# Kernel optimization log

Measured on AMD Instinct MI355X. Metric: run time of the kernel, lower is better.

Reference implementation:

```python
import jax, jax.numpy as jnp
import numpy as np
import math

# D4 group multiplication permutations (rows of the 8x8 regular representation)
PERMS = (
    (0, 1, 2, 3, 4, 5, 6, 7),
    (3, 0, 1, 2, 5, 6, 7, 4),
    (2, 3, 0, 1, 6, 7, 4, 5),
    (1, 2, 3, 0, 7, 4, 5, 6),
    (4, 5, 6, 7, 0, 1, 2, 3),
    (5, 6, 7, 4, 3, 0, 1, 2),
    (6, 7, 4, 5, 2, 3, 0, 1),
    (7, 4, 5, 6, 1, 2, 3, 0),
)


def d4_1x1(x, w):
    """D4-equivariant 1x1 conv. x: (b, cin*8, h, w), w: (cout, cin, 8)."""
    b, C, h, ww = x.shape
    cout, cin, _ = w.shape
    # (cout, 8, cin, 8): permuted copies of the base weight
    W = jnp.stack([w[..., jnp.array(p)] for p in PERMS], axis=1)
    xr = x.reshape(b, cin, 8, h, ww)
    y = jnp.einsum('ogif,bifhw->boghw', W, xr)
    return y.reshape(b, cout * 8, h, ww)


def group_norm(x, gamma, beta, num_groups, eps=1e-5):
    b, C, h, w = x.shape
    xg = x.reshape(b, num_groups, C // num_groups, h, w)
    mean = xg.mean(axis=(2, 3, 4), keepdims=True)
    var = xg.var(axis=(2, 3, 4), keepdims=True)
    xn = ((xg - mean) / jnp.sqrt(var + eps)).reshape(b, C, h, w)
    return xn * gamma[None, :, None, None] + beta[None, :, None, None]


def unfold_patches(x, k):
    """torch.nn.Unfold(k, 1, (k-1)//2, 1) -> (b, C, k*k, h, w), patch idx = ki*k+kj."""
    b, C, h, w = x.shape
    p = (k - 1) // 2
    xp = jnp.pad(x, ((0, 0), (0, 0), (p, p), (p, p)))
    pats = jnp.stack([xp[:, :, i:i + h, j:j + w]
                      for i in range(k) for j in range(k)], axis=2)
    return pats


def setup_inputs() -> dict:
    key = jax.random.key(0)
    ks = jax.random.split(key, 4)
    b, H, W = 8, 56, 56
    cin, cout, rr, k, gc = 64, 64, 2, 3, 16
    cmid = cin // rr            # 32
    G = cout // gc              # 4 dynamic-kernel groups
    x = jax.random.normal(ks[0], (b, cin * 8, H, W), jnp.float32)
    w_v = jax.random.normal(ks[1], (cout, cin, 8), jnp.float32) / math.sqrt(8 * cin / 2)
    w1 = jax.random.normal(ks[2], (cmid, cin, 8), jnp.float32) / math.sqrt(8 * cin / 2)
    gn_gamma = jnp.ones((cmid * 8,), jnp.float32)
    gn_beta = jnp.zeros((cmid * 8,), jnp.float32)
    w2 = jax.random.normal(ks[3], (k * k * G, cmid), jnp.float32) / math.sqrt(cmid)
    b2 = jnp.zeros((k * k * G,), jnp.float32)
    return {"x": x, "w_v": w_v, "w1": w1, "gn_gamma": gn_gamma,
            "gn_beta": gn_beta, "w2": w2, "b2": b2}


def reference(x, w_v, w1, gn_gamma, gn_beta, w2, b2):
    k, gc = 3, 16
    b, _, h, w = x.shape
    cmid = w1.shape[0]
    G = w2.shape[0] // (k * k)
    # --- dynamic kernel branch: conv1 (D4 1x1 + GN + ReLU), conv2 (1x1x1 conv3d)
    t = jax.nn.relu(group_norm(d4_1x1(x, w1), gn_gamma, gn_beta, cmid))
    tr = t.reshape(b, cmid, 8, h, w)
    wgt = jnp.einsum('oi,bighw->boghw', w2, tr) + b2[None, :, None, None, None]
    wv = wgt.reshape(b, G, k, k, 8, h, w)
    # --- D4 symmetrization of the k x k kernel per group element
    s = [wv[:, :, :, :, g] for g in range(8)]          # each (b,G,k,k,h,w)
    sw = [jnp.swapaxes(s[g], 2, 3) for g in range(4, 8)]
    trans = [s[0],
             jnp.rot90(s[1], 1, (2, 3)),
             jnp.rot90(s[2], 2, (2, 3)),
             jnp.rot90(s[3], 3, (2, 3)),
             jnp.rot90(sw[0], 3, (2, 3)),
             jnp.rot90(sw[1], 2, (2, 3)),
             jnp.rot90(sw[2], 1, (2, 3)),
             sw[3]]
    wv = jnp.stack(trans, axis=4)                      # (b,G,k,k,8,h,w)
    wv = wv.reshape(b, G, k * k, 8, h, w)[:, :, None]  # (b,G,1,k^2,8,h,w)
    wv = jnp.swapaxes(wv, 3, 4)                        # (b,G,1,8,k^2,h,w)
    # --- value branch + unfold + multiply-sum
    xv = d4_1x1(x, w_v)                                # (b, cout*8, h, w)
    pats = unfold_patches(xv, k).reshape(b, G, gc, 8, k * k, h, w)
    out = (wv * pats).sum(axis=4)                      # (b,G,gc,8,h,w)
    return out.reshape(b, G * gc * 8, h, w)
```

## Files before the change

kernel.cpp:

```cpp
#include <hip/hip_runtime.h>

#define BATCH 8
#define PIX   3136
#define CIN8  512
#define CMID8 256
#define KDIM  512

typedef short short8 __attribute__((ext_vector_type(8)));
typedef float f32x4 __attribute__((ext_vector_type(4)));

__constant__ int c_perms[8][8] = {
    {0, 1, 2, 3, 4, 5, 6, 7},
    {3, 0, 1, 2, 5, 6, 7, 4},
    {2, 3, 0, 1, 6, 7, 4, 5},
    {1, 2, 3, 0, 7, 4, 5, 6},
    {4, 5, 6, 7, 0, 1, 2, 3},
    {5, 6, 7, 4, 3, 0, 1, 2},
    {6, 7, 4, 5, 2, 3, 0, 1},
};
__constant__ int c_perm7[8] = {7, 4, 5, 6, 1, 2, 3, 0};

__constant__ int c_tab[8][9] = {
    {0, 1, 2, 3, 4, 5, 6, 7, 8},
    {2, 5, 8, 1, 4, 7, 0, 3, 6},
    {8, 7, 6, 5, 4, 3, 2, 1, 0},
    {6, 3, 0, 7, 4, 1, 8, 5, 2},
    {2, 1, 0, 5, 4, 3, 8, 7, 6},
    {8, 5, 2, 7, 4, 1, 6, 3, 0},
    {6, 7, 8, 3, 4, 5, 0, 1, 2},
    {0, 3, 6, 1, 4, 7, 2, 5, 8},
};

__device__ __forceinline__ float bf2f(unsigned short u) {
    union { unsigned int i; float f; } v;
    v.i = ((unsigned int)u) << 16;
    return v.f;
}
__device__ __forceinline__ unsigned short f2bf(float f) {
    union { float f; unsigned int u; } v;
    v.f = f;
    unsigned int u = v.u;
    u += 0x7FFFu + ((u >> 16) & 1u);
    return (unsigned short)(u >> 16);
}
__device__ __forceinline__ float bflo(unsigned int u) {
    union { unsigned int i; float f; } v; v.i = u << 16; return v.f;
}
__device__ __forceinline__ float bfhi(unsigned int u) {
    union { unsigned int i; float f; } v; v.i = u & 0xFFFF0000u; return v.f;
}

__device__ __forceinline__ void gload_lds16(const unsigned short* g, unsigned short* l) {
    __builtin_amdgcn_global_load_lds(
        (const __attribute__((address_space(1))) unsigned int*)g,
        (__attribute__((address_space(3))) unsigned int*)l,
        16, 0, 0);
}

#define LDT 70
__global__ __launch_bounds__(256) void cvt_t_kernel(
    const float* __restrict__ x, unsigned short* __restrict__ xbfT)
{
    __shared__ unsigned short T[64 * LDT];
    const int flat = blockIdx.x;
    const int kt = flat & 7;
    const int pt = (flat >> 3) % 49;
    const int b  = flat / (49 * 8);
    const int k0 = kt * 64, p0 = pt * 64;

    const float* xb = x + ((size_t)b * CIN8 + k0) * PIX + p0;
    const int kl = threadIdx.x >> 4;
    const int pl = (threadIdx.x & 15) * 4;
#pragma unroll
    for (int pass = 0; pass < 4; ++pass) {
        int kk = kl + pass * 16;
        float4 v = *(const float4*)(xb + (size_t)kk * PIX + pl);
        ushort2 lo = {f2bf(v.x), f2bf(v.y)};
        ushort2 hi = {f2bf(v.z), f2bf(v.w)};
        *(ushort2*)&T[kk * LDT + pl]     = lo;
        *(ushort2*)&T[kk * LDT + pl + 2] = hi;
    }
    __syncthreads();
    const int prow = threadIdx.x >> 2;
    const int kc8  = (threadIdx.x & 3) * 8;
    unsigned short* ob = xbfT + ((size_t)b * PIX + p0 + prow) * KDIM + k0;
#pragma unroll
    for (int pass = 0; pass < 2; ++pass) {
        int kk = kc8 + pass * 32;
        unsigned short tmp[8];
#pragma unroll
        for (int j = 0; j < 8; ++j) tmp[j] = T[(kk + j) * LDT + prow];
        *(uint4*)(ob + kk) = *(const uint4*)tmp;
    }
}

__global__ __launch_bounds__(256) void build_w_kernel(
    const float* __restrict__ w_v, const float* __restrict__ w1,
    unsigned short* __restrict__ Wbig, float* __restrict__ stats2)
{
    if (blockIdx.x < 2) stats2[blockIdx.x * 256 + threadIdx.x] = 0.f;

    int idx = blockIdx.x * 256 + threadIdx.x;
    int r = idx >> 9;
    int k = idx & 511;
    int i = k >> 3, f = k & 7;
    float v;
    if (r < 512) {
        int o = r >> 3, g = r & 7;
        int pf = (g < 7) ? c_perms[g][f] : c_perm7[f];
        v = w_v[(o * 64 + i) * 8 + pf];
    } else {
        int rr = r - 512;
        int o = rr >> 3, g = rr & 7;
        int pf = (g < 7) ? c_perms[g][f] : c_perm7[f];
        v = w1[(o * 64 + i) * 8 + pf];
    }
    Wbig[idx] = f2bf(v);
}

__global__ __launch_bounds__(256, 4) void gemm_kernel(
    const unsigned short* __restrict__ xT,
    const unsigned short* __restrict__ Wbig,
    unsigned short* __restrict__ xv,
    unsigned short* __restrict__ y1b,
    float* __restrict__ stats2)
{
    __shared__ unsigned short Wt[128 * 64];
    __shared__ unsigned short Xt[128 * 64];

    const int swz = (blockIdx.x & 7) * 147 + (blockIdx.x >> 3);
    const int rt  = swz % 6;
    const int pt  = swz / 6;
    const int row0 = rt * 128;
    const int P0   = pt * 128;

    const int tid  = threadIdx.x;
    const int lane = tid & 63;
    const int wave = tid >> 6;
    const int wm   = wave & 1;
    const int wn   = wave >> 1;

    f32x4 acc[4][4];
#pragma unroll
    for (int i = 0; i < 4; ++i)
#pragma unroll
        for (int j = 0; j < 4; ++j) acc[i][j] = (f32x4){0.f, 0.f, 0.f, 0.f};

    const int lr  = lane >> 3;
    const int lc  = lane & 7;
    const int swc = ((lc ^ lr) * 8);
    const unsigned short* wsrc = Wbig + (size_t)(row0 + wave * 32 + lr) * KDIM + swc;
    const unsigned short* xsrc = xT + (size_t)(P0 + wave * 32 + lr) * KDIM + swc;
    unsigned short* wdst = &Wt[(wave * 32) * 64];
    unsigned short* xdst = &Xt[(wave * 32) * 64];

    const int m16 = lane & 15;
    const int lq  = lane >> 4;
    const int swr = m16 & 7;

    for (int kc = 0; kc < 8; ++kc) {
        const int k0 = kc * 64;
#pragma unroll
        for (int i = 0; i < 4; ++i) {
            gload_lds16(wsrc + (size_t)i * 8 * KDIM + k0, wdst + i * 512);
            gload_lds16(xsrc + (size_t)i * 8 * KDIM + k0, xdst + i * 512);
        }
        __syncthreads();

#pragma unroll
        for (int kk = 0; kk < 2; ++kk) {
            const int ck = (((kk << 2) | lq) ^ swr) * 8;
            short8 bfrag[4];
#pragma unroll
            for (int nt = 0; nt < 4; ++nt)
                bfrag[nt] = *(const short8*)&Xt[(wn * 64 + nt * 16 + m16) * 64 + ck];
#pragma unroll
            for (int mt = 0; mt < 4; ++mt) {
                short8 afrag = *(const short8*)&Wt[(wm * 64 + mt * 16 + m16) * 64 + ck];
#pragma unroll
                for (int nt = 0; nt < 4; ++nt)
                    acc[mt][nt] = __builtin_amdgcn_mfma_f32_16x16x32_bf16(
                        afrag, bfrag[nt], acc[mt][nt], 0, 0, 0);
            }
        }
        __syncthreads();
    }

    const int colw = P0 + wn * 64;
    const int bb   = colw / PIX;
    const int pq   = colw - bb * PIX;
    const int qm   = lq * 4;

    if (row0 < 512) {
        unsigned short* dst0 = xv + ((size_t)bb * CIN8) * PIX + pq + m16;
#pragma unroll
        for (int nt = 0; nt < 4; ++nt) {
            unsigned short* dst = dst0 + nt * 16;
#pragma unroll
            for (int mt = 0; mt < 4; ++mt) {
                const int m = row0 + wm * 64 + mt * 16 + qm;
#pragma unroll
                for (int r = 0; r < 4; ++r)
                    dst[(size_t)(m + r) * PIX] = f2bf(acc[mt][nt][r]);
            }
        }
    } else {
        unsigned short* dst0 = y1b + ((size_t)bb * CMID8) * PIX + pq + m16;
#pragma unroll
        for (int nt = 0; nt < 4; ++nt) {
            unsigned short* dst = dst0 + nt * 16;
#pragma unroll
            for (int mt = 0; mt < 4; ++mt) {
                const int m = (row0 - 512) + wm * 64 + mt * 16 + qm;
#pragma unroll
                for (int r = 0; r < 4; ++r)
                    dst[(size_t)(m + r) * PIX] = f2bf(acc[mt][nt][r]);
            }
        }
        const int gbase = ((row0 - 512) + wm * 64) >> 3;
#pragma unroll
        for (int mt = 0; mt < 4; ++mt) {
            float s = 0.f, ss = 0.f;
#pragma unroll
            for (int nt = 0; nt < 4; ++nt)
#pragma unroll
                for (int r = 0; r < 4; ++r) {
                    float v = acc[mt][nt][r];
                    s += v; ss += v * v;
                }
#pragma unroll
            for (int off = 1; off <= 16; off <<= 1) {
                s  += __shfl_xor(s, off);
                ss += __shfl_xor(ss, off);
            }
            if ((lane & 31) == 0) {
                const int g = gbase + 2 * mt + (lane >> 5);
                atomicAdd(&stats2[(bb * 32 + g) * 2],     s);
                atomicAdd(&stats2[(bb * 32 + g) * 2 + 1], ss);
            }
        }
    }
}

__global__ __launch_bounds__(256) void final_fused_kernel(
    const unsigned short* __restrict__ y1b, const float* __restrict__ stats2,
    const float* __restrict__ gamma, const float* __restrict__ beta,
    const float* __restrict__ w2, const float* __restrict__ b2,
    const unsigned short* __restrict__ xv,
    float* __restrict__ out)
{
    const int swz  = (blockIdx.x & 7) * 128 + (blockIdx.x >> 3);
    const int combo = swz >> 2;
    const int b    = combo >> 5;
    const int g    = (combo >> 2) & 7;
    const int gidx = combo & 3;

    __shared__ float w2s[9 * 32];
    __shared__ float b2s9[9];
    __shared__ float scs[32], shs[32];
    const int tid = threadIdx.x;
    for (int i = tid; i < 288; i += 256) {
        int tt = i >> 5, ic = i & 31;
        w2s[i] = w2[(gidx * 9 + c_tab[g][tt]) * 32 + ic];
    }
    if (tid < 9) b2s9[tid] = b2[gidx * 9 + c_tab[g][tid]];
    if (tid < 32) {
        float S  = stats2[(b * 32 + tid) * 2];
        float SS = stats2[(b * 32 + tid) * 2 + 1];
        float mean = S * (1.f / 25088.f);
        float var  = SS * (1.f / 25088.f) - mean * mean;
        float rstd = rsqrtf(var + 1e-5f);
        float sc = rstd * gamma[tid * 8 + g];
        scs[tid] = sc;
        shs[tid] = beta[tid * 8 + g] - mean * sc;
    }
    __syncthreads();

    const int pp = (swz & 3) * 256 + tid;
    if (pp >= 784) return;
    const int p0 = pp * 4;
    const int h  = p0 / 56;
    const int w0 = p0 % 56;

    float wt[4][9];
#pragma unroll
    for (int i = 0; i < 4; ++i)
#pragma unroll
        for (int tt = 0; tt < 9; ++tt) wt[i][tt] = b2s9[tt];

    const unsigned short* yb = y1b + ((size_t)b * CMID8 + g) * PIX + p0;
#pragma unroll 4
    for (int ic = 0; ic < 32; ++ic) {
        uint2 u = *(const uint2*)(yb + (size_t)(ic * 8) * PIX);
        float t0 = bflo(u.x) * scs[ic] + shs[ic]; t0 = t0 > 0.f ? t0 : 0.f;
        float t1 = bfhi(u.x) * scs[ic] + shs[ic]; t1 = t1 > 0.f ? t1 : 0.f;
        float t2 = bflo(u.y) * scs[ic] + shs[ic]; t2 = t2 > 0.f ? t2 : 0.f;
        float t3 = bfhi(u.y) * scs[ic] + shs[ic]; t3 = t3 > 0.f ? t3 : 0.f;
#pragma unroll
        for (int tt = 0; tt < 9; ++tt) {
            float wv = w2s[tt * 32 + ic];
            wt[0][tt] = fmaf(wv, t0, wt[0][tt]);
            wt[1][tt] = fmaf(wv, t1, wt[1][tt]);
            wt[2][tt] = fmaf(wv, t2, wt[2][tt]);
            wt[3][tt] = fmaf(wv, t3, wt[3][tt]);
        }
    }

    int rb[3];
#pragma unroll
    for (int ki = 0; ki < 3; ++ki) {
        int hh = h + ki - 1;
        bool rv = (hh >= 0) & (hh < 56);
        int hc = hh < 0 ? 0 : (hh > 55 ? 55 : hh);
        rb[ki] = hc * 56;
        if (!rv) {
#pragma unroll
            for (int i = 0; i < 4; ++i)
#pragma unroll
                for (int kj = 0; kj < 3; ++kj) wt[i][ki * 3 + kj] = 0.f;
        }
    }
#pragma unroll
    for (int i = 0; i < 4; ++i)
#pragma unroll
        for (int tt = 0; tt < 9; ++tt) {
            int ww = w0 + i + (tt % 3) - 1;
            if (ww < 0 || ww >= 56) wt[i][tt] = 0.f;
        }

    const int c0 = (w0 == 0) ? 0 : (w0 - 2);

    const unsigned short* xc = xv + ((size_t)b * CIN8 + gidx * 128 + g) * PIX;
    float* ob = out + ((size_t)b * CIN8 + gidx * 128 + g) * PIX + p0;
#pragma unroll 2
    for (int cc = 0; cc < 16; ++cc) {
        f32x4 a = (f32x4){0.f, 0.f, 0.f, 0.f};
#pragma unroll
        for (int ki = 0; ki < 3; ++ki) {
            const unsigned short* row = xc + rb[ki];
            unsigned int u0 = *(const unsigned int*)(row + c0);
            unsigned int u1 = *(const unsigned int*)(row + w0);
            unsigned int u2 = *(const unsigned int*)(row + w0 + 2);
            unsigned int u3 = *(const unsigned int*)(row + w0 + 4);
            float f1 = bfhi(u0);
            float f2 = bflo(u1), f3 = bfhi(u1);
            float f4 = bflo(u2), f5 = bfhi(u2);
            float f6 = bflo(u3);
            const int t0i = ki * 3;
            a[0] = fmaf(wt[0][t0i + 0], f1, a[0]);
            a[0] = fmaf(wt[0][t0i + 1], f2, a[0]);
            a[0] = fmaf(wt[0][t0i + 2], f3, a[0]);
            a[1] = fmaf(wt[1][t0i + 0], f2, a[1]);
            a[1] = fmaf(wt[1][t0i + 1], f3, a[1]);
            a[1] = fmaf(wt[1][t0i + 2], f4, a[1]);
            a[2] = fmaf(wt[2][t0i + 0], f3, a[2]);
            a[2] = fmaf(wt[2][t0i + 1], f4, a[2]);
            a[2] = fmaf(wt[2][t0i + 2], f5, a[2]);
            a[3] = fmaf(wt[3][t0i + 0], f4, a[3]);
            a[3] = fmaf(wt[3][t0i + 1], f5, a[3]);
            a[3] = fmaf(wt[3][t0i + 2], f6, a[3]);
        }
        *(f32x4*)(ob + (size_t)cc * 8 * PIX) = a;
        xc += (size_t)8 * PIX;
    }
}

extern "C" void kernel_launch(void* const* d_in, const int* in_sizes, int n_in,
                              void* d_out, int out_size, void* d_ws, size_t ws_size,
                              hipStream_t stream) {
    (void)in_sizes; (void)n_in; (void)out_size; (void)ws_size;
    const float* x     = (const float*)d_in[0];
    const float* w_v   = (const float*)d_in[1];
    const float* w1    = (const float*)d_in[2];
    const float* gamma = (const float*)d_in[3];
    const float* beta  = (const float*)d_in[4];
    const float* w2    = (const float*)d_in[5];
    const float* b2    = (const float*)d_in[6];
    float* out = (float*)d_out;

    char* ws = (char*)d_ws;
    unsigned short* Wbig = (unsigned short*)ws;
    unsigned short* xbfT = (unsigned short*)(ws + 786432);
    unsigned short* xv   = (unsigned short*)(ws + 26476544);
    unsigned short* y1b  = (unsigned short*)(ws + 52166656);
    float* stats2 = (float*)(ws + 65011712);

    cvt_t_kernel<<<3136, 256, 0, stream>>>(x, xbfT);
    build_w_kernel<<<1536, 256, 0, stream>>>(w_v, w1, Wbig, stats2);
    gemm_kernel<<<1176, 256, 0, stream>>>(xbfT, Wbig, xv, y1b, stats2);
    final_fused_kernel<<<256 * 4, 256, 0, stream>>>(
        y1b, stats2, gamma, beta, w2, b2, xv, out);
}
```

Baseline: 160.3 us.

## Fuse fp32-to-bf16 transpose of x into GEMM tile loading

Drops the standalone convert/transpose kernel. The GEMM now loads fp32 x directly, converts it to bf16 in registers and writes it transposed into swizzled LDS. This avoids a separate kernel launch and the write and re-read of a bf16 transposed copy of x. In exchange, the GEMM reads twice the bytes per tile, repeated across row tiles, and uses synchronous loads instead of async global-to-LDS loads for that operand.

```diff
diff --git a/kernel.cpp b/kernel.cpp
--- a/kernel.cpp
+++ b/kernel.cpp
@@ -55,43 +55,6 @@
         (const __attribute__((address_space(1))) unsigned int*)g,
         (__attribute__((address_space(3))) unsigned int*)l,
         16, 0, 0);
-}
-
-#define LDT 70
-__global__ __launch_bounds__(256) void cvt_t_kernel(
-    const float* __restrict__ x, unsigned short* __restrict__ xbfT)
-{
-    __shared__ unsigned short T[64 * LDT];
-    const int flat = blockIdx.x;
-    const int kt = flat & 7;
-    const int pt = (flat >> 3) % 49;
-    const int b  = flat / (49 * 8);
-    const int k0 = kt * 64, p0 = pt * 64;
-
-    const float* xb = x + ((size_t)b * CIN8 + k0) * PIX + p0;
-    const int kl = threadIdx.x >> 4;
-    const int pl = (threadIdx.x & 15) * 4;
-#pragma unroll
-    for (int pass = 0; pass < 4; ++pass) {
-        int kk = kl + pass * 16;
-        float4 v = *(const float4*)(xb + (size_t)kk * PIX + pl);
-        ushort2 lo = {f2bf(v.x), f2bf(v.y)};
-        ushort2 hi = {f2bf(v.z), f2bf(v.w)};
-        *(ushort2*)&T[kk * LDT + pl]     = lo;
-        *(ushort2*)&T[kk * LDT + pl + 2] = hi;
-    }
-    __syncthreads();
-    const int prow = threadIdx.x >> 2;
-    const int kc8  = (threadIdx.x & 3) * 8;
-    unsigned short* ob = xbfT + ((size_t)b * PIX + p0 + prow) * KDIM + k0;
-#pragma unroll
-    for (int pass = 0; pass < 2; ++pass) {
-        int kk = kc8 + pass * 32;
-        unsigned short tmp[8];
-#pragma unroll
-        for (int j = 0; j < 8; ++j) tmp[j] = T[(kk + j) * LDT + prow];
-        *(uint4*)(ob + kk) = *(const uint4*)tmp;
-    }
 }
 
 __global__ __launch_bounds__(256) void build_w_kernel(
@@ -119,7 +82,7 @@
 }
 
 __global__ __launch_bounds__(256, 4) void gemm_kernel(
-    const unsigned short* __restrict__ xT,
+    const float* __restrict__ x,
     const unsigned short* __restrict__ Wbig,
     unsigned short* __restrict__ xv,
     unsigned short* __restrict__ y1b,
@@ -150,9 +113,19 @@
     const int lc  = lane & 7;
     const int swc = ((lc ^ lr) * 8);
     const unsigned short* wsrc = Wbig + (size_t)(row0 + wave * 32 + lr) * KDIM + swc;
-    const unsigned short* xsrc = xT + (size_t)(P0 + wave * 32 + lr) * KDIM + swc;
     unsigned short* wdst = &Wt[(wave * 32) * 64];
-    unsigned short* xdst = &Xt[(wave * 32) * 64];
+
+    const int kb = tid & 7;
+    const int pb = tid >> 3;
+    const int colx = P0 + pb * 4;
+    const int bx = colx / PIX;
+    const int px = colx - bx * PIX;
+    const float* xpA = x + ((size_t)bx * CIN8 + kb * 4) * PIX + px;
+    const float* xpB = xpA + (size_t)32 * PIX;
+    const int rowp = pb * 4;
+    const int cA = kb >> 1;
+    const int cB = (kb >> 1) + 4;
+    const int sub4 = (kb & 1) * 4;
 
     const int m16 = lane & 15;
     const int lq  = lane >> 4;
@@ -161,9 +134,26 @@
     for (int kc = 0; kc < 8; ++kc) {
         const int k0 = kc * 64;
 #pragma unroll
-        for (int i = 0; i < 4; ++i) {
+        for (int i = 0; i < 4; ++i)
             gload_lds16(wsrc + (size_t)i * 8 * KDIM + k0, wdst + i * 512);
-            gload_lds16(xsrc + (size_t)i * 8 * KDIM + k0, xdst + i * 512);
+        f32x4 xa[4], xb[4];
+#pragma unroll
+        for (int i = 0; i < 4; ++i)
+            xa[i] = *(const f32x4*)(xpA + (size_t)(k0 + i) * PIX);
+#pragma unroll
+        for (int i = 0; i < 4; ++i)
+            xb[i] = *(const f32x4*)(xpB + (size_t)(k0 + i) * PIX);
+#pragma unroll
+        for (int j = 0; j < 4; ++j) {
+            const int row = rowp + j;
+            const int rx  = row & 7;
+            unsigned int lo, hi;
+            lo = (unsigned int)f2bf(xa[0][j]) | ((unsigned int)f2bf(xa[1][j]) << 16);
+            hi = (unsigned int)f2bf(xa[2][j]) | ((unsigned int)f2bf(xa[3][j]) << 16);
+            *(uint2*)&Xt[row * 64 + (cA ^ rx) * 8 + sub4] = (uint2){lo, hi};
+            lo = (unsigned int)f2bf(xb[0][j]) | ((unsigned int)f2bf(xb[1][j]) << 16);
+            hi = (unsigned int)f2bf(xb[2][j]) | ((unsigned int)f2bf(xb[3][j]) << 16);
+            *(uint2*)&Xt[row * 64 + (cB ^ rx) * 8 + sub4] = (uint2){lo, hi};
         }
         __syncthreads();
 
@@ -380,14 +370,12 @@
 
     char* ws = (char*)d_ws;
     unsigned short* Wbig = (unsigned short*)ws;
-    unsigned short* xbfT = (unsigned short*)(ws + 786432);
-    unsigned short* xv   = (unsigned short*)(ws + 26476544);
-    unsigned short* y1b  = (unsigned short*)(ws + 52166656);
-    float* stats2 = (float*)(ws + 65011712);
-
-    cvt_t_kernel<<<3136, 256, 0, stream>>>(x, xbfT);
+    unsigned short* xv   = (unsigned short*)(ws + 786432);
+    unsigned short* y1b  = (unsigned short*)(ws + 26476544);
+    float* stats2 = (float*)(ws + 39321600);
+
     build_w_kernel<<<1536, 256, 0, stream>>>(w_v, w1, Wbig, stats2);
-    gemm_kernel<<<1176, 256, 0, stream>>>(xbfT, Wbig, xv, y1b, stats2);
+    gemm_kernel<<<1176, 256, 0, stream>>>(x, Wbig, xv, y1b, stats2);
     final_fused_kernel<<<256 * 4, 256, 0, stream>>>(
         y1b, stats2, gamma, beta, w2, b2, xv, out);
 }
```

Result: slower. 186.5 us (+16.4%).

## Double-buffer value-branch rows in LDS with async global-to-LDS prefetch

Applied to the files above, without the earlier changes.

The final fused kernel now stages each channel's needed row band of the value tensor (the block's rows plus a one-row halo) into a double-buffered shared-memory tile. It uses async global-to-LDS loads, prefetching the next channel while the current one is computed. The 3x3 neighbourhood reads then come from LDS instead of repeated, partly redundant global loads. The cost is a block-wide barrier every channel iteration, and inactive threads must stay alive to take part in the loads and barriers, which may limit overlap.

```diff
diff --git a/kernel.cpp b/kernel.cpp
--- a/kernel.cpp
+++ b/kernel.cpp
@@ -242,6 +242,7 @@
     }
 }
 
+#define STG_N 1200
 __global__ __launch_bounds__(256) void final_fused_kernel(
     const unsigned short* __restrict__ y1b, const float* __restrict__ stats2,
     const float* __restrict__ gamma, const float* __restrict__ beta,
@@ -254,10 +255,13 @@
     const int b    = combo >> 5;
     const int g    = (combo >> 2) & 7;
     const int gidx = combo & 3;
+    const int q    = swz & 3;
 
     __shared__ float w2s[9 * 32];
     __shared__ float b2s9[9];
     __shared__ float scs[32], shs[32];
+    __shared__ unsigned short stg[2][STG_N];
+
     const int tid = threadIdx.x;
     for (int i = tid; i < 288; i += 256) {
         int tt = i >> 5, ic = i & 31;
@@ -274,10 +278,22 @@
         scs[tid] = sc;
         shs[tid] = beta[tid * 8 + g] - mean * sc;
     }
+
+    const int P = q * 1024;
+    int rowlo = P / 56 - 1; if (rowlo < 0) rowlo = 0;
+    int rowhi = (P + 1023) / 56 + 1; if (rowhi > 55) rowhi = 55;
+    const int nst = (rowhi - rowlo + 1) * 56;
+    const unsigned short* xcb = xv + ((size_t)b * CIN8 + gidx * 128 + g) * PIX
+                                   + rowlo * 56;
+    const bool doload = (tid * 8) < nst;
+    unsigned short* stdst0 = &stg[0][(tid >> 6) * 512];
+    unsigned short* stdst1 = &stg[1][(tid >> 6) * 512];
+
+    if (doload) gload_lds16(xcb + tid * 8, stdst0);
     __syncthreads();
 
-    const int pp = (swz & 3) * 256 + tid;
-    if (pp >= 784) return;
+    const int pp = q * 256 + tid;
+    const bool act = pp < 784;
     const int p0 = pp * 4;
     const int h  = p0 / 56;
     const int w0 = p0 % 56;
@@ -288,21 +304,23 @@
 #pragma unroll
         for (int tt = 0; tt < 9; ++tt) wt[i][tt] = b2s9[tt];
 
-    const unsigned short* yb = y1b + ((size_t)b * CMID8 + g) * PIX + p0;
+    if (act) {
+        const unsigned short* yb = y1b + ((size_t)b * CMID8 + g) * PIX + p0;
 #pragma unroll 4
-    for (int ic = 0; ic < 32; ++ic) {
-        uint2 u = *(const uint2*)(yb + (size_t)(ic * 8) * PIX);
-        float t0 = bflo(u.x) * scs[ic] + shs[ic]; t0 = t0 > 0.f ? t0 : 0.f;
-        float t1 = bfhi(u.x) * scs[ic] + shs[ic]; t1 = t1 > 0.f ? t1 : 0.f;
-        float t2 = bflo(u.y) * scs[ic] + shs[ic]; t2 = t2 > 0.f ? t2 : 0.f;
-        float t3 = bfhi(u.y) * scs[ic] + shs[ic]; t3 = t3 > 0.f ? t3 : 0.f;
-#pragma unroll
-        for (int tt = 0; tt < 9; ++tt) {
-            float wv = w2s[tt * 32 + ic];
-            wt[0][tt] = fmaf(wv, t0, wt[0][tt]);
-            wt[1][tt] = fmaf(wv, t1, wt[1][tt]);
-            wt[2][tt] = fmaf(wv, t2, wt[2][tt]);
-            wt[3][tt] = fmaf(wv, t3, wt[3][tt]);
+        for (int ic = 0; ic < 32; ++ic) {
+            uint2 u = *(const uint2*)(yb + (size_t)(ic * 8) * PIX);
+            float t0 = bflo(u.x) * scs[ic] + shs[ic]; t0 = t0 > 0.f ? t0 : 0.f;
+            float t1 = bfhi(u.x) * scs[ic] + shs[ic]; t1 = t1 > 0.f ? t1 : 0.f;
+            float t2 = bflo(u.y) * scs[ic] + shs[ic]; t2 = t2 > 0.f ? t2 : 0.f;
+            float t3 = bfhi(u.y) * scs[ic] + shs[ic]; t3 = t3 > 0.f ? t3 : 0.f;
+#pragma unroll
+            for (int tt = 0; tt < 9; ++tt) {
+                float wv = w2s[tt * 32 + ic];
+                wt[0][tt] = fmaf(wv, t0, wt[0][tt]);
+                wt[1][tt] = fmaf(wv, t1, wt[1][tt]);
+                wt[2][tt] = fmaf(wv, t2, wt[2][tt]);
+                wt[3][tt] = fmaf(wv, t3, wt[3][tt]);
+            }
         }
     }
 
@@ -312,7 +330,8 @@
         int hh = h + ki - 1;
         bool rv = (hh >= 0) & (hh < 56);
         int hc = hh < 0 ? 0 : (hh > 55 ? 55 : hh);
-        rb[ki] = hc * 56;
+        rb[ki] = (hc - rowlo) * 56;
+        if (rb[ki] < 0) rb[ki] = 0;
         if (!rv) {
 #pragma unroll
             for (int i = 0; i < 4; ++i)
@@ -330,38 +349,44 @@
 
     const int c0 = (w0 == 0) ? 0 : (w0 - 2);
 
-    const unsigned short* xc = xv + ((size_t)b * CIN8 + gidx * 128 + g) * PIX;
     float* ob = out + ((size_t)b * CIN8 + gidx * 128 + g) * PIX + p0;
-#pragma unroll 2
+    int buf = 0;
     for (int cc = 0; cc < 16; ++cc) {
-        f32x4 a = (f32x4){0.f, 0.f, 0.f, 0.f};
-#pragma unroll
-        for (int ki = 0; ki < 3; ++ki) {
-            const unsigned short* row = xc + rb[ki];
-            unsigned int u0 = *(const unsigned int*)(row + c0);
-            unsigned int u1 = *(const unsigned int*)(row + w0);
-            unsigned int u2 = *(const unsigned int*)(row + w0 + 2);
-            unsigned int u3 = *(const unsigned int*)(row + w0 + 4);
-            float f1 = bfhi(u0);
-            float f2 = bflo(u1), f3 = bfhi(u1);
-            float f4 = bflo(u2), f5 = bfhi(u2);
-            float f6 = bflo(u3);
-            const int t0i = ki * 3;
-            a[0] = fmaf(wt[0][t0i + 0], f1, a[0]);
-            a[0] = fmaf(wt[0][t0i + 1], f2, a[0]);
-            a[0] = fmaf(wt[0][t0i + 2], f3, a[0]);
-            a[1] = fmaf(wt[1][t0i + 0], f2, a[1]);
-            a[1] = fmaf(wt[1][t0i + 1], f3, a[1]);
-            a[1] = fmaf(wt[1][t0i + 2], f4, a[1]);
-            a[2] = fmaf(wt[2][t0i + 0], f3, a[2]);
-            a[2] = fmaf(wt[2][t0i + 1], f4, a[2]);
-            a[2] = fmaf(wt[2][t0i + 2], f5, a[2]);
-            a[3] = fmaf(wt[3][t0i + 0], f4, a[3]);
-            a[3] = fmaf(wt[3][t0i + 1], f5, a[3]);
-            a[3] = fmaf(wt[3][t0i + 2], f6, a[3]);
-        }
-        *(f32x4*)(ob + (size_t)cc * 8 * PIX) = a;
-        xc += (size_t)8 * PIX;
+        if (cc < 15 && doload)
+            gload_lds16(xcb + (size_t)(cc + 1) * 8 * PIX + tid * 8,
+                        buf ? stdst0 : stdst1);
+        if (act) {
+            const unsigned short* sb = stg[buf];
+            f32x4 a = (f32x4){0.f, 0.f, 0.f, 0.f};
+#pragma unroll
+            for (int ki = 0; ki < 3; ++ki) {
+                const unsigned short* row = sb + rb[ki];
+                unsigned int u0 = *(const unsigned int*)(row + c0);
+                unsigned int u1 = *(const unsigned int*)(row + w0);
+                unsigned int u2 = *(const unsigned int*)(row + w0 + 2);
+                unsigned int u3 = *(const unsigned int*)(row + w0 + 4);
+                float f1 = bfhi(u0);
+                float f2 = bflo(u1), f3 = bfhi(u1);
+                float f4 = bflo(u2), f5 = bfhi(u2);
+                float f6 = bflo(u3);
+                const int t0i = ki * 3;
+                a[0] = fmaf(wt[0][t0i + 0], f1, a[0]);
+                a[0] = fmaf(wt[0][t0i + 1], f2, a[0]);
+                a[0] = fmaf(wt[0][t0i + 2], f3, a[0]);
+                a[1] = fmaf(wt[1][t0i + 0], f2, a[1]);
+                a[1] = fmaf(wt[1][t0i + 1], f3, a[1]);
+                a[1] = fmaf(wt[1][t0i + 2], f4, a[1]);
+                a[2] = fmaf(wt[2][t0i + 0], f3, a[2]);
+                a[2] = fmaf(wt[2][t0i + 1], f4, a[2]);
+                a[2] = fmaf(wt[2][t0i + 2], f5, a[2]);
+                a[3] = fmaf(wt[3][t0i + 0], f4, a[3]);
+                a[3] = fmaf(wt[3][t0i + 1], f5, a[3]);
+                a[3] = fmaf(wt[3][t0i + 2], f6, a[3]);
+            }
+            *(f32x4*)(ob + (size_t)cc * 8 * PIX) = a;
+        }
+        __syncthreads();
+        buf ^= 1;
     }
 }
 
```

Result: slower. 168.3 us (+5.0%).
